# Kernel tuning notes

Measured on AMD Instinct MI355X. Metric: run time of the kernel, lower is better.

The kernel has to match this reference:

```python
import jax, jax.numpy as jnp
import numpy as np

B, T, C = 512, 256, 384  # batch, seq (<= block_size 256), n_embed
HEAD = 64


def setup_inputs() -> dict:
    key = jax.random.key(0)
    k1, k2, k3, k4 = jax.random.split(key, 4)
    scale = 1.0 / np.sqrt(C)
    return {
        "x": jax.random.normal(k1, (B, T, C), dtype=jnp.float32),
        "Wq": jax.random.normal(k2, (C, HEAD), dtype=jnp.float32) * scale,
        "Wk": jax.random.normal(k3, (C, HEAD), dtype=jnp.float32) * scale,
        "Wv": jax.random.normal(k4, (C, HEAD), dtype=jnp.float32) * scale,
    }


def reference(x, Wq, Wk, Wv):
    # Single causal self-attention head (dropout in eval mode / identity).
    _, T_, C_ = x.shape
    q = x @ Wq  # [B,T,H]
    k = x @ Wk  # [B,T,H]
    v = x @ Wv  # [B,T,H]
    # NOTE: original scales by n_embed**-0.5 (C), not head_size**-0.5.
    wei = jnp.einsum('bth,bsh->bts', q, k) * (C_ ** -0.5)  # [B,T,T]
    causal = jnp.tril(jnp.ones((T_, T_), dtype=bool))
    wei = jnp.where(causal, wei, -jnp.inf)
    wei = jax.nn.softmax(wei, axis=-1)
    return jnp.einsum('bts,bsh->bth', wei, v)  # [B,T,H]
```

## Files before the change

### kernel.cpp

```cpp
#include <hip/hip_runtime.h>

#define B_ 512
#define T_ 256
#define C_ 384
#define H_ 64

typedef __attribute__((ext_vector_type(8))) short bf16x8;
typedef __attribute__((ext_vector_type(4))) float f32x4;

__device__ __forceinline__ short f2bf(float f) {
    unsigned u = __float_as_uint(f);
    u += 0x7fffu + ((u >> 16) & 1u);
    return (short)(u >> 16);
}

__device__ __forceinline__ bf16x8 cvt8(const float* p) {
    const float4* p4 = (const float4*)p;
    float4 a = p4[0], b = p4[1];
    bf16x8 r;
    r[0] = f2bf(a.x); r[1] = f2bf(a.y); r[2] = f2bf(a.z); r[3] = f2bf(a.w);
    r[4] = f2bf(b.x); r[5] = f2bf(b.y); r[6] = f2bf(b.z); r[7] = f2bf(b.w);
    return r;
}

__global__ void pack_w_kernel(const float* __restrict__ Wq, const float* __restrict__ Wk,
                              const float* __restrict__ Wv, short* __restrict__ wp) {
    int p = blockIdx.x * 256 + threadIdx.x;
    if (p >= 12 * 12 * 512) return;
    int j    = p & 7;
    int lane = (p >> 3) & 63;
    int pc   = p >> 9;
    int ct = pc % 12, ks = pc / 12;
    int n  = ct * 16 + (lane & 15);
    int kk = ks * 32 + (lane >> 4) * 8 + j;
    const float* src = (n < 64) ? Wq : ((n < 128) ? Wk : Wv);
    wp[p] = f2bf(src[kk * 64 + (n & 63)]);
}

__global__ __launch_bounds__(256, 2) void qkv_kernel(
    const float* __restrict__ x, const short* __restrict__ wp,
    short* __restrict__ qo, short* __restrict__ ko, short* __restrict__ vo) {
    const int tid  = threadIdx.x;
    const int lane = tid & 63, w = tid >> 6;
    const int cl = lane & 15, quad = lane >> 4;
    const int rowbase = blockIdx.x * 128;

    const float* xr0 = x + (long)(rowbase + w * 32 + cl) * C_;
    const float* xr1 = xr0 + 16 * C_;

    f32x4 acc[2][12];
    #pragma unroll
    for (int rt = 0; rt < 2; rt++)
        #pragma unroll
        for (int ct = 0; ct < 12; ct++) {
            f32x4 z = {0.f, 0.f, 0.f, 0.f};
            acc[rt][ct] = z;
        }

    const short* wl = wp + lane * 8;
    for (int ks = 0; ks < 12; ks++) {
        const int koff = ks * 32 + quad * 8;
        bf16x8 a0 = cvt8(xr0 + koff);
        bf16x8 a1 = cvt8(xr1 + koff);
        const short* wk = wl + ks * 6144;
        #pragma unroll
        for (int ct = 0; ct < 12; ct++) {
            bf16x8 bf = *(const bf16x8*)(wk + ct * 512);
            acc[0][ct] = __builtin_amdgcn_mfma_f32_16x16x32_bf16(a0, bf, acc[0][ct], 0, 0, 0);
            acc[1][ct] = __builtin_amdgcn_mfma_f32_16x16x32_bf16(a1, bf, acc[1][ct], 0, 0, 0);
        }
    }

    #pragma unroll
    for (int rt = 0; rt < 2; rt++) {
        const int gb = rowbase + w * 32 + rt * 16 + quad * 4;
        #pragma unroll
        for (int ct = 0; ct < 12; ct++) {
            const int n = ct * 16 + cl;
            short* dstp = (n < 64) ? qo : ((n < 128) ? ko : vo);
            const int nn = n & 63;
            #pragma unroll
            for (int r = 0; r < 4; r++)
                dstp[(long)(gb + r) * 64 + nn] = f2bf(acc[rt][ct][r]);
        }
    }
}

__global__ __launch_bounds__(256, 3) void attn_kernel(
    const short* __restrict__ qi, const short* __restrict__ ki,
    const short* __restrict__ vi, float* __restrict__ out) {
    __shared__ short Vs[64 * 264];
    __shared__ short Pb[4][16 * 40];

    const int b = blockIdx.x >> 1;
    const int ph = blockIdx.x & 1;
    const int tid = threadIdx.x;
    const int w = tid >> 6, lane = tid & 63;
    const int cl = lane & 15, quad = lane >> 4;

    const short* vb = vi + b * (T_ * H_);
    for (int i = tid; i < (T_ * H_ / 4); i += 256) {
        const int h = i & 63, tg = i >> 6;
        short4 val;
        val.x = vb[(tg * 4 + 0) * 64 + h];
        val.y = vb[(tg * 4 + 1) * 64 + h];
        val.z = vb[(tg * 4 + 2) * 64 + h];
        val.w = vb[(tg * 4 + 3) * 64 + h];
        *(short4*)(Vs + h * 264 + tg * 4) = val;
    }
    __syncthreads();

    const float scale = 0.05103103630798287f;

    for (int it = 0; it < 2; it++) {
        const int rg0 = ph * 4 + w;
        const int rg = it ? (15 - rg0) : rg0;
        const int base = rg << 4;

        const short* qb = qi + (long)(b * T_ + base + cl) * H_;
        const bf16x8 qf0 = *(const bf16x8*)(qb + quad * 8);
        const bf16x8 qf1 = *(const bf16x8*)(qb + 32 + quad * 8);

        f32x4 sacc[16];
        #pragma unroll
        for (int st = 0; st < 16; st++) {
            if (st > rg) continue;
            const short* kb = ki + (long)(b * T_ + st * 16 + cl) * H_;
            bf16x8 k0 = *(const bf16x8*)(kb + quad * 8);
            bf16x8 k1 = *(const bf16x8*)(kb + 32 + quad * 8);
            f32x4 z = {0.f, 0.f, 0.f, 0.f};
            f32x4 t = __builtin_amdgcn_mfma_f32_16x16x32_bf16(qf0, k0, z, 0, 0, 0);
            t = __builtin_amdgcn_mfma_f32_16x16x32_bf16(qf1, k1, t, 0, 0, 0);
            sacc[st] = t;
        }

        float m4[4] = {-3e38f, -3e38f, -3e38f, -3e38f};
        #pragma unroll
        for (int st = 0; st < 16; st++) {
            if (st > rg) continue;
            #pragma unroll
            for (int r = 0; r < 4; r++) {
                float sv = sacc[st][r] * scale;
                if (st * 16 + cl > base + quad * 4 + r) sv = -1e30f;
                sacc[st][r] = sv;
                m4[r] = fmaxf(m4[r], sv);
            }
        }
        #pragma unroll
        for (int d = 1; d < 16; d <<= 1)
            #pragma unroll
            for (int r = 0; r < 4; r++)
                m4[r] = fmaxf(m4[r], __shfl_xor(m4[r], d));

        float l4[4] = {0.f, 0.f, 0.f, 0.f};
        #pragma unroll
        for (int st = 0; st < 16; st++) {
            if (st > rg) continue;
            #pragma unroll
            for (int r = 0; r < 4; r++) {
                float pv = exp2f((sacc[st][r] - m4[r]) * 1.4426950408889634f);
                sacc[st][r] = pv;
                l4[r] += pv;
            }
        }
        #pragma unroll
        for (int d = 1; d < 16; d <<= 1)
            #pragma unroll
            for (int r = 0; r < 4; r++)
                l4[r] += __shfl_xor(l4[r], d);

        f32x4 oacc[4];
        #pragma unroll
        for (int ht = 0; ht < 4; ht++) {
            f32x4 z = {0.f, 0.f, 0.f, 0.f};
            oacc[ht] = z;
        }
        short* pb = Pb[w];
        #pragma unroll
        for (int c = 0; c < 8; c++) {
            if (c > (rg >> 1)) continue;
            #pragma unroll
            for (int half = 0; half < 2; half++) {
                const int st = c * 2 + half;
                #pragma unroll
                for (int r = 0; r < 4; r++) {
                    short pv = (st <= rg) ? f2bf(sacc[st][r]) : (short)0;
                    pb[(quad * 4 + r) * 40 + half * 16 + cl] = pv;
                }
            }
            __builtin_amdgcn_wave_barrier();
            const bf16x8 pa = *(const bf16x8*)(pb + cl * 40 + quad * 8);
            #pragma unroll
            for (int ht = 0; ht < 4; ht++) {
                const bf16x8 vf = *(const bf16x8*)(Vs + (ht * 16 + cl) * 264 + c * 32 + quad * 8);
                oacc[ht] = __builtin_amdgcn_mfma_f32_16x16x32_bf16(pa, vf, oacc[ht], 0, 0, 0);
            }
            __builtin_amdgcn_wave_barrier();
        }

        #pragma unroll
        for (int r = 0; r < 4; r++) {
            const float inv = 1.0f / l4[r];
            float* op = out + (long)(b * T_ + base + quad * 4 + r) * H_ + cl;
            #pragma unroll
            for (int ht = 0; ht < 4; ht++)
                op[ht * 16] = oacc[ht][r] * inv;
        }
    }
}

extern "C" void kernel_launch(void* const* d_in, const int* in_sizes, int n_in,
                              void* d_out, int out_size, void* d_ws, size_t ws_size,
                              hipStream_t stream) {
    const float* x  = (const float*)d_in[0];
    const float* Wq = (const float*)d_in[1];
    const float* Wk = (const float*)d_in[2];
    const float* Wv = (const float*)d_in[3];
    float* out = (float*)d_out;

    short* ws = (short*)d_ws;
    const long QKV = (long)B_ * T_ * H_;
    short* q  = ws;
    short* k  = ws + QKV;
    short* v  = ws + 2 * QKV;
    short* wp = ws + 3 * QKV;

    pack_w_kernel<<<288, 256, 0, stream>>>(Wq, Wk, Wv, wp);
    qkv_kernel<<<(B_ * T_) / 128, 256, 0, stream>>>(x, wp, q, k, v);
    attn_kernel<<<B_ * 2, 256, 0, stream>>>(q, k, v, out);
}
```

Before: 357.7 us.

## Fuse QKV projection and causal attention into one per-batch kernel

Merges the QKV projection and attention kernels into a single kernel with one 512-thread block per batch. Each block computes Q, K and V for its 256 rows and keeps K and V in shared memory, laid out to match the MFMA fragment layout, while Q is converted to register fragments. This removes the global round-trip of the bf16 Q/K/V tensors and one kernel launch. In exchange the grid drops to 512 larger blocks and shared memory use per block grows, which may lower occupancy.

```diff
diff --git a/kernel.cpp b/kernel.cpp
--- a/kernel.cpp
+++ b/kernel.cpp
@@ -37,16 +37,23 @@
     wp[p] = f2bf(src[kk * 64 + (n & 63)]);
 }
 
-__global__ __launch_bounds__(256, 2) void qkv_kernel(
+__global__ __launch_bounds__(512, 2) void fused_kernel(
     const float* __restrict__ x, const short* __restrict__ wp,
-    short* __restrict__ qo, short* __restrict__ ko, short* __restrict__ vo) {
-    const int tid  = threadIdx.x;
-    const int lane = tid & 63, w = tid >> 6;
+    float* __restrict__ out) {
+    __shared__ short Ks[32 * 512];
+    __shared__ short Vs[32 * 512];
+    __shared__ short Pb[8][16 * 40];
+
+    const int b = blockIdx.x;
+    const int tid = threadIdx.x;
+    const int w = tid >> 6, lane = tid & 63;
     const int cl = lane & 15, quad = lane >> 4;
-    const int rowbase = blockIdx.x * 128;
-
-    const float* xr0 = x + (long)(rowbase + w * 32 + cl) * C_;
-    const float* xr1 = xr0 + 16 * C_;
+
+    const float* xb = x + (long)b * (T_ * C_);
+    const int r0 = 16 * w;
+    const int r1 = 240 - 16 * w;
+    const float* xr0 = xb + (long)(r0 + cl) * C_;
+    const float* xr1 = xb + (long)(r1 + cl) * C_;
 
     f32x4 acc[2][12];
     #pragma unroll
@@ -73,61 +80,65 @@
 
     #pragma unroll
     for (int rt = 0; rt < 2; rt++) {
-        const int gb = rowbase + w * 32 + rt * 16 + quad * 4;
-        #pragma unroll
-        for (int ct = 0; ct < 12; ct++) {
-            const int n = ct * 16 + cl;
-            short* dstp = (n < 64) ? qo : ((n < 128) ? ko : vo);
-            const int nn = n & 63;
-            #pragma unroll
-            for (int r = 0; r < 4; r++)
-                dstp[(long)(gb + r) * 64 + nn] = f2bf(acc[rt][ct][r]);
+        const int tb = (rt ? r1 : r0) + quad * 4;
+        #pragma unroll
+        for (int ct = 4; ct < 8; ct++) {
+            const int h = (ct - 4) * 16 + cl;
+            const int kk = h >> 5, hq = (h & 31) >> 3, j = h & 7;
+            #pragma unroll
+            for (int r = 0; r < 4; r++) {
+                const int t = tb + r;
+                Ks[((t >> 4) * 2 + kk) * 512 + ((t & 15) + 16 * hq) * 8 + j] =
+                    f2bf(acc[rt][ct][r]);
+            }
+        }
+        #pragma unroll
+        for (int ct = 8; ct < 12; ct++) {
+            const int ht = ct - 8;
+            #pragma unroll
+            for (int r = 0; r < 4; r++) {
+                const int t = tb + r;
+                Vs[((t >> 5) * 4 + ht) * 512 + (cl + 16 * ((t >> 3) & 3)) * 8 + (t & 7)] =
+                    f2bf(acc[rt][ct][r]);
+            }
         }
     }
-}
-
-__global__ __launch_bounds__(256, 3) void attn_kernel(
-    const short* __restrict__ qi, const short* __restrict__ ki,
-    const short* __restrict__ vi, float* __restrict__ out) {
-    __shared__ short Vs[64 * 264];
-    __shared__ short Pb[4][16 * 40];
-
-    const int b = blockIdx.x >> 1;
-    const int ph = blockIdx.x & 1;
-    const int tid = threadIdx.x;
-    const int w = tid >> 6, lane = tid & 63;
-    const int cl = lane & 15, quad = lane >> 4;
-
-    const short* vb = vi + b * (T_ * H_);
-    for (int i = tid; i < (T_ * H_ / 4); i += 256) {
-        const int h = i & 63, tg = i >> 6;
-        short4 val;
-        val.x = vb[(tg * 4 + 0) * 64 + h];
-        val.y = vb[(tg * 4 + 1) * 64 + h];
-        val.z = vb[(tg * 4 + 2) * 64 + h];
-        val.w = vb[(tg * 4 + 3) * 64 + h];
-        *(short4*)(Vs + h * 264 + tg * 4) = val;
-    }
+
+    short* pb = Pb[w];
+    bf16x8 qf[2][2];
+    #pragma unroll
+    for (int rt = 0; rt < 2; rt++)
+        #pragma unroll
+        for (int kk = 0; kk < 2; kk++) {
+            #pragma unroll
+            for (int cth = 0; cth < 2; cth++) {
+                const int ct = kk * 2 + cth;
+                #pragma unroll
+                for (int r = 0; r < 4; r++)
+                    pb[(quad * 4 + r) * 40 + cth * 16 + cl] = f2bf(acc[rt][ct][r]);
+            }
+            __builtin_amdgcn_wave_barrier();
+            qf[rt][kk] = *(const bf16x8*)(pb + cl * 40 + quad * 8);
+            __builtin_amdgcn_wave_barrier();
+        }
+
     __syncthreads();
 
     const float scale = 0.05103103630798287f;
 
+    #pragma unroll
     for (int it = 0; it < 2; it++) {
-        const int rg0 = ph * 4 + w;
-        const int rg = it ? (15 - rg0) : rg0;
+        const int rg = it ? (15 - w) : w;
         const int base = rg << 4;
-
-        const short* qb = qi + (long)(b * T_ + base + cl) * H_;
-        const bf16x8 qf0 = *(const bf16x8*)(qb + quad * 8);
-        const bf16x8 qf1 = *(const bf16x8*)(qb + 32 + quad * 8);
+        const bf16x8 qf0 = qf[it][0];
+        const bf16x8 qf1 = qf[it][1];
 
         f32x4 sacc[16];
         #pragma unroll
         for (int st = 0; st < 16; st++) {
             if (st > rg) continue;
-            const short* kb = ki + (long)(b * T_ + st * 16 + cl) * H_;
-            bf16x8 k0 = *(const bf16x8*)(kb + quad * 8);
-            bf16x8 k1 = *(const bf16x8*)(kb + 32 + quad * 8);
+            bf16x8 k0 = *(const bf16x8*)(Ks + (st * 2 + 0) * 512 + lane * 8);
+            bf16x8 k1 = *(const bf16x8*)(Ks + (st * 2 + 1) * 512 + lane * 8);
             f32x4 z = {0.f, 0.f, 0.f, 0.f};
             f32x4 t = __builtin_amdgcn_mfma_f32_16x16x32_bf16(qf0, k0, z, 0, 0, 0);
             t = __builtin_amdgcn_mfma_f32_16x16x32_bf16(qf1, k1, t, 0, 0, 0);
@@ -175,7 +186,6 @@
             f32x4 z = {0.f, 0.f, 0.f, 0.f};
             oacc[ht] = z;
         }
-        short* pb = Pb[w];
         #pragma unroll
         for (int c = 0; c < 8; c++) {
             if (c > (rg >> 1)) continue;
@@ -192,7 +202,7 @@
             const bf16x8 pa = *(const bf16x8*)(pb + cl * 40 + quad * 8);
             #pragma unroll
             for (int ht = 0; ht < 4; ht++) {
-                const bf16x8 vf = *(const bf16x8*)(Vs + (ht * 16 + cl) * 264 + c * 32 + quad * 8);
+                const bf16x8 vf = *(const bf16x8*)(Vs + (c * 4 + ht) * 512 + lane * 8);
                 oacc[ht] = __builtin_amdgcn_mfma_f32_16x16x32_bf16(pa, vf, oacc[ht], 0, 0, 0);
             }
             __builtin_amdgcn_wave_barrier();
@@ -218,14 +228,8 @@
     const float* Wv = (const float*)d_in[3];
     float* out = (float*)d_out;
 
-    short* ws = (short*)d_ws;
-    const long QKV = (long)B_ * T_ * H_;
-    short* q  = ws;
-    short* k  = ws + QKV;
-    short* v  = ws + 2 * QKV;
-    short* wp = ws + 3 * QKV;
+    short* wp = (short*)d_ws;
 
     pack_w_kernel<<<288, 256, 0, stream>>>(Wq, Wk, Wv, wp);
-    qkv_kernel<<<(B_ * T_) / 128, 256, 0, stream>>>(x, wp, q, k, v);
-    attn_kernel<<<B_ * 2, 256, 0, stream>>>(q, k, v, out);
-}
+    fused_kernel<<<B_, 512, 0, stream>>>(x, wp, out);
+}
```

Measured after the change: 325.5 us. -9.0%, faster.
